# Kernel optimization log

Hardware: AMD Instinct MI355X
Metric: run time of the kernel (lower is better)

## Reference

```python
import jax, jax.numpy as jnp
import numpy as np


def _sample_plane(plane, coords):
    """torch.nn.functional.grid_sample, mode='bilinear', padding_mode='zeros',
    align_corners=True.  plane: [C,H,W]; coords: [N,2] with (x,y) in [-1,1]
    (x indexes W, y indexes H, as in torch grid convention).  Returns [N,C]."""
    C, H, W = plane.shape
    x = (coords[:, 0] + 1.0) * 0.5 * (W - 1)
    y = (coords[:, 1] + 1.0) * 0.5 * (H - 1)
    x0f = jnp.floor(x); y0f = jnp.floor(y)
    wx = x - x0f; wy = y - y0f

    def corner(yi, xi):
        valid = (xi >= 0) & (xi < W) & (yi >= 0) & (yi < H)
        xc = jnp.clip(xi, 0, W - 1).astype(jnp.int32)
        yc = jnp.clip(yi, 0, H - 1).astype(jnp.int32)
        return plane[:, yc, xc] * valid.astype(plane.dtype)  # [C,N]

    v00 = corner(y0f, x0f)
    v01 = corner(y0f, x0f + 1)
    v10 = corner(y0f + 1, x0f)
    v11 = corner(y0f + 1, x0f + 1)
    out = (v00 * (1 - wx) * (1 - wy) + v01 * wx * (1 - wy)
           + v10 * (1 - wx) * wy + v11 * wx * wy)
    return out.T  # [N,C]


_sample_batched = jax.vmap(_sample_plane)  # [B,C,H,W],[B,N,2] -> [B,N,C]


def setup_inputs() -> dict:
    key = jax.random.key(0)
    ks = jax.random.split(key, 8)
    B, N, C, R = 4, 131072, 32, 256
    triplanes = jax.random.normal(ks[0], (B, 3, C, R, R), jnp.float32) * 0.1
    coordinates = jax.random.uniform(ks[1], (B, N, 3), jnp.float32, -1.0, 1.0)
    # MLP weights ~ frequency_init(30) / first_layer_sine_init scales
    w0 = jax.random.uniform(ks[2], (128, C), jnp.float32, -1.0 / C, 1.0 / C)
    b0 = jnp.zeros((128,), jnp.float32)
    s1 = np.sqrt(6.0 / 128) / 30.0
    w1 = jax.random.uniform(ks[3], (128, 128), jnp.float32, -s1, s1)
    b1 = jnp.zeros((128,), jnp.float32)
    w2 = jax.random.uniform(ks[4], (1, 128), jnp.float32, -s1, s1)
    b2 = jnp.zeros((1,), jnp.float32)
    return {"triplanes": triplanes, "coordinates": coordinates,
            "w0": w0, "b0": b0, "w1": w1, "b1": b1, "w2": w2, "b2": b2}


def reference(triplanes, coordinates, w0, b0, w1, b1, w2, b2):
    # triplanes: [B,3,C,R,R]; coordinates: [B,N,3]
    xy = _sample_batched(triplanes[:, 0], coordinates[..., 0:2])   # (x,y)
    yz = _sample_batched(triplanes[:, 1], coordinates[..., 1:3])   # (y,z)
    xz = _sample_batched(triplanes[:, 2], coordinates[..., 0::2])  # (x,z)
    features = xy * yz * xz  # aggregate_fn == 'prod'; [B,N,C]
    h = jax.nn.relu(jnp.einsum('bnc,hc->bnh', features, w0) + b0)
    h = jax.nn.relu(jnp.einsum('bnh,gh->bng', h, w1) + b1)
    return jnp.einsum('bng,og->bno', h, w2) + b2  # [B,N,1]
```

## Files before the change

### kernel.cpp

```cpp
#include <hip/hip_runtime.h>
#include <hip/hip_bf16.h>
#include <cstddef>

#define RES 256
#define NCH 32
#define NPT 131072
#define NB  4

typedef _Float16 half8 __attribute__((ext_vector_type(8)));
typedef _Float16 half4 __attribute__((ext_vector_type(4)));
typedef float    f32x4 __attribute__((ext_vector_type(4)));

#define FEAT_STRIDE 40
#define H0_STRIDE   136

__global__ __launch_bounds__(256) void transpose_fp16_kernel(
    const float* __restrict__ in, _Float16* __restrict__ out)
{
    __shared__ _Float16 tileh[NCH][RES + 8];
    const int bp = blockIdx.y;
    const int y  = blockIdx.x;
    const int t  = threadIdx.x;

    const float4* src4 = (const float4*)(in + (size_t)bp * NCH * RES * RES);
    const int lane64 = t & 63;
    const int cq     = t >> 6;
    #pragma unroll
    for (int i = 0; i < 8; ++i) {
        const int c = cq * 8 + i;
        const float4 v = src4[(size_t)c * (RES * RES / 4) + y * (RES / 4) + lane64];
        half4 h = { (_Float16)v.x, (_Float16)v.y, (_Float16)v.z, (_Float16)v.w };
        *(half4*)&tileh[c][lane64 * 4] = h;
    }
    __syncthreads();

    _Float16* dst = out + ((size_t)bp * RES * RES + (size_t)y * RES) * NCH;
    const int x = t;
    #pragma unroll
    for (int cg = 0; cg < 4; ++cg) {
        half8 h;
        #pragma unroll
        for (int k = 0; k < 8; ++k)
            h[k] = tileh[cg * 8 + k][x];
        *(half8*)&dst[(size_t)x * NCH + cg * 8] = h;
    }
}

__global__ __launch_bounds__(256) void prep_weights(
    const float* __restrict__ w0, const float* __restrict__ w1,
    _Float16* __restrict__ w0h, _Float16* __restrict__ w1h)
{
    const int i = blockIdx.x * 256 + threadIdx.x;
    if (i < 128 * NCH) w0h[i] = (_Float16)(w0[i] * 16.0f);
    if (i < 128 * 128) w1h[i] = (_Float16)w1[i];
}

__global__ __launch_bounds__(256, 2) void fused_kernel(
    const _Float16* __restrict__ planesT,
    const float* __restrict__ coords,
    const _Float16* __restrict__ w0h,
    const _Float16* __restrict__ w1h,
    const float* __restrict__ b0, const float* __restrict__ b1,
    const float* __restrict__ w2, const float* __restrict__ b2,
    float* __restrict__ out)
{
    __shared__ __align__(16) _Float16 smem[4 * 32 * H0_STRIDE];
    _Float16* featLDS = smem;
    _Float16* h0LDS   = smem;

    const int tid  = threadIdx.x;
    const int wv   = tid >> 6;
    const int lane = tid & 63;
    const int l15  = lane & 15;
    const int quad = lane >> 4;

    {
        const int p  = tid >> 1;
        const int hf = tid & 1;
        const int gp = blockIdx.x * 128 + p;
        const int b  = gp >> 17;
        const float cx = coords[(size_t)gp * 3 + 0];
        const float cy = coords[(size_t)gp * 3 + 1];
        const float cz = coords[(size_t)gp * 3 + 2];

        float f[3][16];
        #pragma unroll
        for (int pl = 0; pl < 3; ++pl) {
            const float u = (pl == 0) ? cx : (pl == 1) ? cy : cx;
            const float v = (pl == 0) ? cy : cz;

            const float fx = (u + 1.0f) * 0.5f * (RES - 1);
            const float fy = (v + 1.0f) * 0.5f * (RES - 1);
            const float x0f = floorf(fx), y0f = floorf(fy);
            const float wx = fx - x0f, wy = fy - y0f;
            const int x0 = (int)x0f, y0 = (int)y0f;
            const bool vx1 = (x0 + 1) < RES;
            const bool vy1 = (y0 + 1) < RES;
            const int x1 = vx1 ? x0 + 1 : RES - 1;
            const int y1 = vy1 ? y0 + 1 : RES - 1;

            float w00 = (1.0f - wx) * (1.0f - wy);
            float w01 = wx * (1.0f - wy);
            float w10 = (1.0f - wx) * wy;
            float w11 = wx * wy;
            if (!vx1) { w01 = 0.0f; w11 = 0.0f; }
            if (!vy1) { w10 = 0.0f; w11 = 0.0f; }

            const _Float16* base = planesT
                + ((size_t)(b * 3 + pl) * RES * RES) * NCH + hf * 16;

            const half8* p00 = (const half8*)(base + (size_t)(y0 * RES + x0) * NCH);
            const half8* p01 = (const half8*)(base + (size_t)(y0 * RES + x1) * NCH);
            const half8* p10 = (const half8*)(base + (size_t)(y1 * RES + x0) * NCH);
            const half8* p11 = (const half8*)(base + (size_t)(y1 * RES + x1) * NCH);

            const half8 a00 = p00[0], b00 = p00[1];
            const half8 a01 = p01[0], b01 = p01[1];
            const half8 a10 = p10[0], b10 = p10[1];
            const half8 a11 = p11[0], b11 = p11[1];

            #pragma unroll
            for (int k = 0; k < 8; ++k) {
                f[pl][k] = fmaf((float)a11[k], w11, fmaf((float)a10[k], w10,
                           fmaf((float)a01[k], w01, (float)a00[k] * w00)));
                f[pl][8 + k] = fmaf((float)b11[k], w11, fmaf((float)b10[k], w10,
                               fmaf((float)b01[k], w01, (float)b00[k] * w00)));
            }
        }
        half8 o0, o1;
        #pragma unroll
        for (int k = 0; k < 8; ++k) {
            o0[k] = (_Float16)(f[0][k]     * f[1][k]     * f[2][k]     * 256.0f);
            o1[k] = (_Float16)(f[0][8 + k] * f[1][8 + k] * f[2][8 + k] * 256.0f);
        }
        *(half8*)&featLDS[p * FEAT_STRIDE + hf * 16 + 0] = o0;
        *(half8*)&featLDS[p * FEAT_STRIDE + hf * 16 + 8] = o1;
    }

    const int m0l = wv * 32;

    half8 a0[2];
    #pragma unroll
    for (int mt = 0; mt < 2; ++mt)
        a0[mt] = *(const half8*)&featLDS[(m0l + mt * 16 + l15) * FEAT_STRIDE + quad * 8];

    __syncthreads();

    float b0v[8], b1v[8], w2s[8];
    #pragma unroll
    for (int nt = 0; nt < 8; ++nt) {
        b0v[nt] = b0[nt * 16 + l15] * 4096.0f;
        b1v[nt] = b1[nt * 16 + l15] * 4096.0f;
        w2s[nt] = w2[nt * 16 + l15] * (1.0f / 4096.0f);
    }

    _Float16* h0w = h0LDS + wv * 32 * H0_STRIDE;

    #pragma unroll 1
    for (int nt = 0; nt < 8; ++nt) {
        const half8 bfr = *(const half8*)&w0h[(nt * 16 + l15) * NCH + quad * 8];
        f32x4 acc[2];
        #pragma unroll
        for (int mt = 0; mt < 2; ++mt) {
            acc[mt] = (f32x4){0.f, 0.f, 0.f, 0.f};
            acc[mt] = __builtin_amdgcn_mfma_f32_16x16x32_f16(
                a0[mt], bfr, acc[mt], 0, 0, 0);
        }
        #pragma unroll
        for (int mt = 0; mt < 2; ++mt)
            #pragma unroll
            for (int r = 0; r < 4; ++r) {
                const float hval = fmaxf(acc[mt][r] + b0v[nt], 0.0f);
                h0w[(mt * 16 + quad * 4 + r) * H0_STRIDE + nt * 16 + l15]
                    = (_Float16)hval;
            }
    }

    half8 a1[2][4];
    #pragma unroll
    for (int mt = 0; mt < 2; ++mt)
        #pragma unroll
        for (int ks = 0; ks < 4; ++ks)
            a1[mt][ks] = *(const half8*)
                &h0w[(mt * 16 + l15) * H0_STRIDE + ks * 32 + quad * 8];

    float part[2][4];
    #pragma unroll
    for (int mt = 0; mt < 2; ++mt)
        #pragma unroll
        for (int r = 0; r < 4; ++r) part[mt][r] = 0.0f;

    #pragma unroll 1
    for (int nt = 0; nt < 8; ++nt) {
        f32x4 acc[2];
        #pragma unroll
        for (int mt = 0; mt < 2; ++mt) acc[mt] = (f32x4){0.f, 0.f, 0.f, 0.f};
        #pragma unroll
        for (int ks = 0; ks < 4; ++ks) {
            const half8 bfr = *(const half8*)
                &w1h[(nt * 16 + l15) * 128 + ks * 32 + quad * 8];
            #pragma unroll
            for (int mt = 0; mt < 2; ++mt)
                acc[mt] = __builtin_amdgcn_mfma_f32_16x16x32_f16(
                    a1[mt][ks], bfr, acc[mt], 0, 0, 0);
        }
        #pragma unroll
        for (int mt = 0; mt < 2; ++mt)
            #pragma unroll
            for (int r = 0; r < 4; ++r)
                part[mt][r] = fmaf(w2s[nt], fmaxf(acc[mt][r] + b1v[nt], 0.0f),
                                   part[mt][r]);
    }

    #pragma unroll
    for (int mt = 0; mt < 2; ++mt)
        #pragma unroll
        for (int r = 0; r < 4; ++r) {
            float s = part[mt][r];
            s += __shfl_xor(s, 1);
            s += __shfl_xor(s, 2);
            s += __shfl_xor(s, 4);
            s += __shfl_xor(s, 8);
            part[mt][r] = s;
        }

    if (l15 == 0) {
        const float bias2 = b2[0];
        const int base = blockIdx.x * 128 + m0l;
        #pragma unroll
        for (int mt = 0; mt < 2; ++mt)
            #pragma unroll
            for (int r = 0; r < 4; ++r)
                out[base + mt * 16 + quad * 4 + r] = part[mt][r] + bias2;
    }
}

__global__ __launch_bounds__(256) void fused_fallback(
    const float* __restrict__ planes, const float* __restrict__ coords,
    const float* __restrict__ w0, const float* __restrict__ b0,
    const float* __restrict__ w1, const float* __restrict__ b1,
    const float* __restrict__ w2, const float* __restrict__ b2,
    float* __restrict__ out)
{
    const int t = blockIdx.x * 256 + threadIdx.x;
    const int b = t >> 17;
    const float cx = coords[(size_t)t * 3 + 0];
    const float cy = coords[(size_t)t * 3 + 1];
    const float cz = coords[(size_t)t * 3 + 2];
    float feat[NCH];
    #pragma unroll
    for (int p = 0; p < 3; ++p) {
        const float u = (p == 0) ? cx : (p == 1) ? cy : cx;
        const float v = (p == 0) ? cy : cz;
        const float fx = (u + 1.0f) * 0.5f * (RES - 1);
        const float fy = (v + 1.0f) * 0.5f * (RES - 1);
        const float x0f = floorf(fx), y0f = floorf(fy);
        const float wx = fx - x0f, wy = fy - y0f;
        const int x0 = (int)x0f, y0 = (int)y0f;
        const bool vx1 = (x0 + 1) < RES, vy1 = (y0 + 1) < RES;
        const int x1 = vx1 ? x0 + 1 : RES - 1;
        const int y1 = vy1 ? y0 + 1 : RES - 1;
        float w00 = (1.0f - wx) * (1.0f - wy), w01 = wx * (1.0f - wy);
        float w10 = (1.0f - wx) * wy, w11 = wx * wy;
        if (!vx1) { w01 = 0.0f; w11 = 0.0f; }
        if (!vy1) { w10 = 0.0f; w11 = 0.0f; }
        const float* base = planes + (size_t)(b * 3 + p) * NCH * RES * RES;
        const float* p00 = base + (size_t)y0 * RES + x0;
        const float* p01 = base + (size_t)y0 * RES + x1;
        const float* p10 = base + (size_t)y1 * RES + x0;
        const float* p11 = base + (size_t)y1 * RES + x1;
        #pragma unroll
        for (int c = 0; c < NCH; ++c) {
            const size_t off = (size_t)c * RES * RES;
            float s = p00[off] * w00;
            s = fmaf(p01[off], w01, s);
            s = fmaf(p10[off], w10, s);
            s = fmaf(p11[off], w11, s);
            if (p == 0) feat[c] = s; else feat[c] *= s;
        }
    }
    float h0[128];
    #pragma unroll
    for (int g = 0; g < 128; ++g) {
        const float* wr = w0 + g * NCH;
        float aA = b0[g], aB = 0.0f;
        #pragma unroll
        for (int c = 0; c < NCH; c += 2) {
            aA = fmaf(wr[c], feat[c], aA);
            aB = fmaf(wr[c + 1], feat[c + 1], aB);
        }
        h0[g] = fmaxf(aA + aB, 0.0f);
    }
    float o = b2[0];
    for (int g = 0; g < 128; ++g) {
        const float* wr = w1 + g * 128;
        float aA = b1[g], aB = 0.0f, aC = 0.0f, aD = 0.0f;
        #pragma unroll
        for (int h = 0; h < 128; h += 4) {
            aA = fmaf(wr[h], h0[h], aA);
            aB = fmaf(wr[h + 1], h0[h + 1], aB);
            aC = fmaf(wr[h + 2], h0[h + 2], aC);
            aD = fmaf(wr[h + 3], h0[h + 3], aD);
        }
        o = fmaf(fmaxf((aA + aB) + (aC + aD), 0.0f), w2[g], o);
    }
    out[t] = o;
}

extern "C" void kernel_launch(void* const* d_in, const int* in_sizes, int n_in,
                              void* d_out, int out_size, void* d_ws, size_t ws_size,
                              hipStream_t stream)
{
    const float* trip   = (const float*)d_in[0];
    const float* coords = (const float*)d_in[1];
    const float* w0     = (const float*)d_in[2];
    const float* b0     = (const float*)d_in[3];
    const float* w1     = (const float*)d_in[4];
    const float* b1     = (const float*)d_in[5];
    const float* w2     = (const float*)d_in[6];
    const float* b2     = (const float*)d_in[7];
    float* out = (float*)d_out;

    const size_t planesTBytes = (size_t)NB * 3 * RES * RES * NCH * 2;
    const size_t w0hBytes = 128 * NCH * 2;
    const size_t w1hBytes = 128 * 128 * 2;
    const size_t needed = planesTBytes + w0hBytes + w1hBytes;

    if (ws_size >= needed) {
        _Float16* planesT = (_Float16*)d_ws;
        _Float16* w0h     = (_Float16*)((char*)d_ws + planesTBytes);
        _Float16* w1h     = (_Float16*)((char*)d_ws + planesTBytes + w0hBytes);

        transpose_fp16_kernel<<<dim3(RES, NB * 3), 256, 0, stream>>>(trip, planesT);
        prep_weights<<<64, 256, 0, stream>>>(w0, w1, w0h, w1h);
        fused_kernel<<<(NB * NPT) / 128, 256, 0, stream>>>(
            planesT, coords, w0h, w1h, b0, b1, w2, b2, out);
    } else {
        fused_fallback<<<(NB * NPT) / 256, 256, 0, stream>>>(
            trip, coords, w0, b0, w1, b1, w2, b2, out);
    }
}
```

Before: 300.8 us.

## Merge weight prep into transpose kernel and drop block barrier via per-wave LDS

Folds the weight fp16 conversion into the plane transpose launch as an extra grid row, removing one kernel launch. In the fused kernel, each wave now owns a private LDS region for its 32 points' features and hidden activations, so the block-wide __syncthreads between feature writes and MFMA operand loads is removed. The second-layer loop is also unrolled by two. The barrier removal depends on each wave only reading features written by its own lanes (points p&31 map to the same wave), which holds because two threads per point share a wave.

Measured after the change: 296.2 us. No clear change (-1.5%).

```diff
diff --git a/kernel.cpp b/kernel.cpp
--- a/kernel.cpp
+++ b/kernel.cpp
@@ -13,14 +13,26 @@
 
 #define FEAT_STRIDE 40
 #define H0_STRIDE   136
-
-__global__ __launch_bounds__(256) void transpose_fp16_kernel(
-    const float* __restrict__ in, _Float16* __restrict__ out)
+#define WAVE_LDS    (32 * H0_STRIDE)
+
+__global__ __launch_bounds__(256) void transpose_prep_kernel(
+    const float* __restrict__ in,
+    const float* __restrict__ w0, const float* __restrict__ w1,
+    _Float16* __restrict__ out,
+    _Float16* __restrict__ w0h, _Float16* __restrict__ w1h)
 {
+    const int bp = blockIdx.y;
+    const int t  = threadIdx.x;
+
+    if (bp == 12) {
+        const int i = blockIdx.x * 256 + t;
+        if (i < 128 * NCH)  w0h[i] = (_Float16)(w0[i] * 16.0f);
+        if (i < 128 * 128)  w1h[i] = (_Float16)w1[i];
+        return;
+    }
+
     __shared__ _Float16 tileh[NCH][RES + 8];
-    const int bp = blockIdx.y;
-    const int y  = blockIdx.x;
-    const int t  = threadIdx.x;
+    const int y = blockIdx.x;
 
     const float4* src4 = (const float4*)(in + (size_t)bp * NCH * RES * RES);
     const int lane64 = t & 63;
@@ -44,15 +56,6 @@
             h[k] = tileh[cg * 8 + k][x];
         *(half8*)&dst[(size_t)x * NCH + cg * 8] = h;
     }
-}
-
-__global__ __launch_bounds__(256) void prep_weights(
-    const float* __restrict__ w0, const float* __restrict__ w1,
-    _Float16* __restrict__ w0h, _Float16* __restrict__ w1h)
-{
-    const int i = blockIdx.x * 256 + threadIdx.x;
-    if (i < 128 * NCH) w0h[i] = (_Float16)(w0[i] * 16.0f);
-    if (i < 128 * 128) w1h[i] = (_Float16)w1[i];
 }
 
 __global__ __launch_bounds__(256, 2) void fused_kernel(
@@ -64,9 +67,7 @@
     const float* __restrict__ w2, const float* __restrict__ b2,
     float* __restrict__ out)
 {
-    __shared__ __align__(16) _Float16 smem[4 * 32 * H0_STRIDE];
-    _Float16* featLDS = smem;
-    _Float16* h0LDS   = smem;
+    __shared__ __align__(16) _Float16 smem[4 * WAVE_LDS];
 
     const int tid  = threadIdx.x;
     const int wv   = tid >> 6;
@@ -74,8 +75,11 @@
     const int l15  = lane & 15;
     const int quad = lane >> 4;
 
+    _Float16* wbase = smem + wv * WAVE_LDS;
+
     {
         const int p  = tid >> 1;
+        const int pl_ = p & 31;
         const int hf = tid & 1;
         const int gp = blockIdx.x * 128 + p;
         const int b  = gp >> 17;
@@ -133,18 +137,14 @@
             o0[k] = (_Float16)(f[0][k]     * f[1][k]     * f[2][k]     * 256.0f);
             o1[k] = (_Float16)(f[0][8 + k] * f[1][8 + k] * f[2][8 + k] * 256.0f);
         }
-        *(half8*)&featLDS[p * FEAT_STRIDE + hf * 16 + 0] = o0;
-        *(half8*)&featLDS[p * FEAT_STRIDE + hf * 16 + 8] = o1;
-    }
-
-    const int m0l = wv * 32;
+        *(half8*)&wbase[pl_ * FEAT_STRIDE + hf * 16 + 0] = o0;
+        *(half8*)&wbase[pl_ * FEAT_STRIDE + hf * 16 + 8] = o1;
+    }
 
     half8 a0[2];
     #pragma unroll
     for (int mt = 0; mt < 2; ++mt)
-        a0[mt] = *(const half8*)&featLDS[(m0l + mt * 16 + l15) * FEAT_STRIDE + quad * 8];
-
-    __syncthreads();
+        a0[mt] = *(const half8*)&wbase[(mt * 16 + l15) * FEAT_STRIDE + quad * 8];
 
     float b0v[8], b1v[8], w2s[8];
     #pragma unroll
@@ -154,8 +154,6 @@
         w2s[nt] = w2[nt * 16 + l15] * (1.0f / 4096.0f);
     }
 
-    _Float16* h0w = h0LDS + wv * 32 * H0_STRIDE;
-
     #pragma unroll 1
     for (int nt = 0; nt < 8; ++nt) {
         const half8 bfr = *(const half8*)&w0h[(nt * 16 + l15) * NCH + quad * 8];
@@ -171,7 +169,7 @@
             #pragma unroll
             for (int r = 0; r < 4; ++r) {
                 const float hval = fmaxf(acc[mt][r] + b0v[nt], 0.0f);
-                h0w[(mt * 16 + quad * 4 + r) * H0_STRIDE + nt * 16 + l15]
+                wbase[(mt * 16 + quad * 4 + r) * H0_STRIDE + nt * 16 + l15]
                     = (_Float16)hval;
             }
     }
@@ -182,7 +180,7 @@
         #pragma unroll
         for (int ks = 0; ks < 4; ++ks)
             a1[mt][ks] = *(const half8*)
-                &h0w[(mt * 16 + l15) * H0_STRIDE + ks * 32 + quad * 8];
+                &wbase[(mt * 16 + l15) * H0_STRIDE + ks * 32 + quad * 8];
 
     float part[2][4];
     #pragma unroll
@@ -190,7 +188,7 @@
         #pragma unroll
         for (int r = 0; r < 4; ++r) part[mt][r] = 0.0f;
 
-    #pragma unroll 1
+    #pragma unroll 2
     for (int nt = 0; nt < 8; ++nt) {
         f32x4 acc[2];
         #pragma unroll
@@ -226,7 +224,7 @@
 
     if (l15 == 0) {
         const float bias2 = b2[0];
-        const int base = blockIdx.x * 128 + m0l;
+        const int base = blockIdx.x * 128 + wv * 32;
         #pragma unroll
         for (int mt = 0; mt < 2; ++mt)
             #pragma unroll
@@ -331,8 +329,8 @@
         _Float16* w0h     = (_Float16*)((char*)d_ws + planesTBytes);
         _Float16* w1h     = (_Float16*)((char*)d_ws + planesTBytes + w0hBytes);
 
-        transpose_fp16_kernel<<<dim3(RES, NB * 3), 256, 0, stream>>>(trip, planesT);
-        prep_weights<<<64, 256, 0, stream>>>(w0, w1, w0h, w1h);
+        transpose_prep_kernel<<<dim3(RES, NB * 3 + 1), 256, 0, stream>>>(
+            trip, w0, w1, planesT, w0h, w1h);
         fused_kernel<<<(NB * NPT) / 128, 256, 0, stream>>>(
             planesT, coords, w0h, w1h, b0, b1, w2, b2, out);
     } else {
```
